# Kernel optimization log

Measured on AMD Instinct MI355X. Metric: run time of the kernel, lower is better.

Reference implementation:

```python
import jax, jax.numpy as jnp
import numpy as np

ALPHA = 0.1  # LeakyReLU slope

def _leaky(v):
    return jnp.where(v >= 0, v, ALPHA * v)

def setup_inputs() -> dict:
    key = jax.random.key(0)
    k1, k2, k3 = jax.random.split(key, 3)
    B, D_IN, D1, D2 = 262144, 200, 150, 100
    x = jax.random.normal(k1, (B, D_IN), dtype=jnp.float32)
    W1 = jax.random.normal(k2, (D_IN, D1), dtype=jnp.float32) * 0.05
    b1 = jnp.zeros((D1,), dtype=jnp.float32)
    W2 = jax.random.normal(k3, (D1, D2), dtype=jnp.float32) * 0.05
    b2 = jnp.zeros((D2,), dtype=jnp.float32)
    return {"x": x, "W1": W1, "b1": b1, "W2": W2, "b2": b2}

def reference(x, W1, b1, W2, b2):
    # Original loops per sample: dense(200->150)+LeakyReLU, mean -> out1;
    # dense(150->100)+LeakyReLU, mean -> out2. Batched here as single GEMMs.
    h1 = _leaky(x @ W1 + b1)           # [B, 150]
    out1 = jnp.mean(h1, axis=-1)       # [B]
    h2 = _leaky(h1 @ W2 + b2)          # [B, 100]
    out2 = jnp.mean(h2, axis=-1)       # [B]
    return (out1, out2)
```

## Files before the change

### kernel.cpp

```cpp
#include <hip/hip_runtime.h>

typedef unsigned short u16;
typedef unsigned int u32;
typedef __bf16 bf16x8 __attribute__((ext_vector_type(8)));
typedef float f32x4 __attribute__((ext_vector_type(4)));

#define W2F_OFF 71680
#define B1_OFF 107520
#define B2_OFF 108160
#define WS_BYTES 108608

__device__ __align__(256) unsigned char g_wbuf[WS_BYTES];

__device__ __forceinline__ u16 f2bf(float f) {
  __bf16 b = (__bf16)f;
  return __builtin_bit_cast(u16, b);
}
__device__ __forceinline__ u32 pk2bf(float a, float b) {
  return (u32)f2bf(a) | ((u32)f2bf(b) << 16);
}

__global__ void prep_kernel(const float* __restrict__ W1, const float* __restrict__ b1,
                            const float* __restrict__ W2, const float* __restrict__ b2)
{
  const int stride = gridDim.x * blockDim.x;
  const int tid0 = blockIdx.x * blockDim.x + threadIdx.x;
  u16* w1f = (u16*)g_wbuf;
  for (int e = tid0; e < 35840; e += stride) {
    int j = e & 7, l = (e >> 3) & 63, nt = (e >> 9) % 10, kt = e / 5120;
    int k = kt * 32 + ((l >> 4) << 3) + j;
    int n = nt * 16 + (l & 15);
    w1f[e] = (k < 200 && n < 150) ? f2bf(W1[k * 150 + n]) : (u16)0;
  }
  u16* w2f = (u16*)(g_wbuf + W2F_OFF);
  for (int e = tid0; e < 17920; e += stride) {
    int j = e & 7, l = (e >> 3) & 63, nt = (e >> 9) % 7, kt = e / 3584;
    int k = kt * 32 + ((l >> 4) << 3) + j;
    int n = nt * 16 + (l & 15);
    w2f[e] = (k < 150 && n < 100) ? f2bf(W2[k * 100 + n]) : (u16)0;
  }
  float* b1p = (float*)(g_wbuf + B1_OFF);
  for (int e = tid0; e < 160; e += stride) b1p[e] = (e < 150) ? b1[e] : 0.f;
  float* b2p = (float*)(g_wbuf + B2_OFF);
  for (int e = tid0; e < 112; e += stride) b2p[e] = (e < 100) ? b2[e] : 0.f;
}

__global__ __launch_bounds__(256, 5)
void fused_mlp(const float* __restrict__ x, float* __restrict__ out, int B)
{
  __shared__ __align__(16) u16 xs[12800];
  __shared__ float ps[2][2][64];

  const int tid = threadIdx.x;
  const int lane = tid & 63;
  const int wv = tid >> 6;
  const int h = wv & 1;
  const int pr = wv >> 1;
  const int cl = lane & 15, gr = lane >> 4;
  const long r0 = (long)blockIdx.x * 64;

  const u16* w1g = (const u16*)g_wbuf;
  const u16* w2g = (const u16*)(g_wbuf + W2F_OFF);

  const float* xg = x + r0 * 200;
  #pragma unroll
  for (int i = 0; i < 13; ++i) {
    int c = tid + i * 256;
    if (c < 3200) {
      int row = c / 50, kc = c % 50;
      float4 v = *reinterpret_cast<const float4*>(xg + row * 200 + kc * 4);
      int k0 = kc * 4;
      int mt = row >> 4;
      int idx;
      if (k0 < 192) {
        int F = mt * 6 + (k0 >> 5);
        int fl = (row & 15) | (((k0 & 31) >> 3) << 4);
        int slot = fl ^ (F & 7);
        idx = (F * 64 + slot) * 8 + (k0 & 7);
      } else {
        idx = 12288 + mt * 128 + (row & 15) * 8 + (k0 - 192);
      }
      uint2 p;
      p.x = pk2bf(v.x, v.y);
      p.y = pk2bf(v.z, v.w);
      *reinterpret_cast<uint2*>(&xs[idx]) = p;
    }
  }

  bf16x8 bfr[5];
  #pragma unroll
  for (int nt = 0; nt < 5; ++nt)
    bfr[nt] = *reinterpret_cast<const bf16x8*>(w1g + ((0 * 10 + 5 * h + nt) * 64 + lane) * 8);

  __syncthreads();

  const int mt0 = pr * 2, mt1 = pr * 2 + 1;
  const f32x4 zz = {0.f, 0.f, 0.f, 0.f};
  f32x4 acc1[2][5];
  #pragma unroll
  for (int i = 0; i < 2; ++i)
    #pragma unroll
    for (int nt = 0; nt < 5; ++nt) acc1[i][nt] = zz;

  #pragma unroll
  for (int kt = 0; kt < 7; ++kt) {
    bf16x8 a0, a1;
    if (kt < 6) {
      int F0 = mt0 * 6 + kt, F1 = mt1 * 6 + kt;
      a0 = *reinterpret_cast<const bf16x8*>(&xs[(F0 * 64 + (lane ^ (F0 & 7))) * 8]);
      a1 = *reinterpret_cast<const bf16x8*>(&xs[(F1 * 64 + (lane ^ (F1 & 7))) * 8]);
    } else {
      union { bf16x8 v; u32 w[4]; } A0, A1;
      A0.v = *reinterpret_cast<const bf16x8*>(&xs[12288 + mt0 * 128 + cl * 8]);
      A1.v = *reinterpret_cast<const bf16x8*>(&xs[12288 + mt1 * 128 + cl * 8]);
      if (gr != 0) {
        A0.w[0] = A0.w[1] = A0.w[2] = A0.w[3] = 0u;
        A1.w[0] = A1.w[1] = A1.w[2] = A1.w[3] = 0u;
      }
      a0 = A0.v; a1 = A1.v;
    }
    #pragma unroll
    for (int nt = 0; nt < 5; ++nt) {
      bf16x8 b = (kt == 0) ? bfr[nt]
        : *reinterpret_cast<const bf16x8*>(w1g + ((kt * 10 + 5 * h + nt) * 64 + lane) * 8);
      acc1[0][nt] = __builtin_amdgcn_mfma_f32_16x16x32_bf16(a0, b, acc1[0][nt], 0, 0, 0);
      acc1[1][nt] = __builtin_amdgcn_mfma_f32_16x16x32_bf16(a1, b, acc1[1][nt], 0, 0, 0);
    }
  }
  __syncthreads();

  const float* b1p = (const float*)(g_wbuf + B1_OFF);
  float b1v[5];
  #pragma unroll
  for (int nt = 0; nt < 5; ++nt) b1v[nt] = b1p[(5 * h + nt) * 16 + cl];

  float rs0[4] = {0, 0, 0, 0}, rs1[4] = {0, 0, 0, 0};
  #pragma unroll
  for (int nt = 0; nt < 5; ++nt) {
    int k2 = (5 * h + nt) * 16 + cl;
    int kt2 = k2 >> 5;
    int l2base = 16 * ((k2 & 31) >> 3);
    int e2 = k2 & 7;
    #pragma unroll
    for (int j = 0; j < 4; ++j) {
      int l2 = gr * 4 + j + l2base;
      float hv = acc1[0][nt][j] + b1v[nt];
      hv = (hv >= 0.f) ? hv : 0.1f * hv;
      rs0[j] += hv;
      xs[((mt0 * 5 + kt2) * 64 + l2) * 8 + e2] = f2bf(hv);
      float gv = acc1[1][nt][j] + b1v[nt];
      gv = (gv >= 0.f) ? gv : 0.1f * gv;
      rs1[j] += gv;
      xs[((mt1 * 5 + kt2) * 64 + l2) * 8 + e2] = f2bf(gv);
    }
  }
  #pragma unroll
  for (int j = 0; j < 4; ++j) {
    float s0 = rs0[j], s1 = rs1[j];
    #pragma unroll
    for (int mask = 1; mask < 16; mask <<= 1) {
      s0 += __shfl_xor(s0, mask, 64);
      s1 += __shfl_xor(s1, mask, 64);
    }
    if (cl == 0) {
      ps[0][h][mt0 * 16 + gr * 4 + j] = s0;
      ps[0][h][mt1 * 16 + gr * 4 + j] = s1;
    }
  }
  __syncthreads();

  if (wv == 0)
    out[r0 + lane] = (ps[0][0][lane] + ps[0][1][lane]) * (1.f / 150.f);

  f32x4 acc2[2][4];
  #pragma unroll
  for (int i = 0; i < 2; ++i)
    #pragma unroll
    for (int nt = 0; nt < 4; ++nt) acc2[i][nt] = zz;

  #pragma unroll
  for (int kt = 0; kt < 5; ++kt) {
    bf16x8 a0 = *reinterpret_cast<const bf16x8*>(&xs[((mt0 * 5 + kt) * 64 + lane) * 8]);
    bf16x8 a1 = *reinterpret_cast<const bf16x8*>(&xs[((mt1 * 5 + kt) * 64 + lane) * 8]);
    #pragma unroll
    for (int nt = 0; nt < 4; ++nt) {
      if (nt < 3 || h == 0) {
        bf16x8 b = *reinterpret_cast<const bf16x8*>(w2g + ((kt * 7 + 4 * h + nt) * 64 + lane) * 8);
        acc2[0][nt] = __builtin_amdgcn_mfma_f32_16x16x32_bf16(a0, b, acc2[0][nt], 0, 0, 0);
        acc2[1][nt] = __builtin_amdgcn_mfma_f32_16x16x32_bf16(a1, b, acc2[1][nt], 0, 0, 0);
      }
    }
  }

  const float* b2p = (const float*)(g_wbuf + B2_OFF);
  float b2v[4];
  #pragma unroll
  for (int nt = 0; nt < 4; ++nt)
    b2v[nt] = (nt < 3 || h == 0) ? b2p[(4 * h + nt) * 16 + cl] : 0.f;

  float t0[4] = {0, 0, 0, 0}, t1[4] = {0, 0, 0, 0};
  #pragma unroll
  for (int nt = 0; nt < 4; ++nt) {
    if (nt < 3 || h == 0) {
      #pragma unroll
      for (int j = 0; j < 4; ++j) {
        float hv = acc2[0][nt][j] + b2v[nt];
        hv = (hv >= 0.f) ? hv : 0.1f * hv;
        t0[j] += hv;
        float gv = acc2[1][nt][j] + b2v[nt];
        gv = (gv >= 0.f) ? gv : 0.1f * gv;
        t1[j] += gv;
      }
    }
  }
  #pragma unroll
  for (int j = 0; j < 4; ++j) {
    float s0 = t0[j], s1 = t1[j];
    #pragma unroll
    for (int mask = 1; mask < 16; mask <<= 1) {
      s0 += __shfl_xor(s0, mask, 64);
      s1 += __shfl_xor(s1, mask, 64);
    }
    if (cl == 0) {
      ps[1][h][mt0 * 16 + gr * 4 + j] = s0;
      ps[1][h][mt1 * 16 + gr * 4 + j] = s1;
    }
  }
  __syncthreads();

  if (wv == 0)
    out[B + r0 + lane] = (ps[1][0][lane] + ps[1][1][lane]) * (1.f / 100.f);
}

extern "C" void kernel_launch(void* const* d_in, const int* in_sizes, int n_in,
                              void* d_out, int out_size, void* d_ws, size_t ws_size,
                              hipStream_t stream)
{
  const float* x  = (const float*)d_in[0];
  const float* W1 = (const float*)d_in[1];
  const float* b1 = (const float*)d_in[2];
  const float* W2 = (const float*)d_in[3];
  const float* b2 = (const float*)d_in[4];
  float* out = (float*)d_out;
  const int B = in_sizes[0] / 200;

  prep_kernel<<<64, 256, 0, stream>>>(W1, b1, W2, b2);
  fused_mlp<<<B / 64, 256, 0, stream>>>(x, out, B);
}
```

Measured before the change: 80.41 us.

## Make fused MLP blocks loop over eight row tiles with LDS weights and prefetch

After: 88.87 us. 10.5% more time.

```diff
diff --git a/kernel.cpp b/kernel.cpp
--- a/kernel.cpp
+++ b/kernel.cpp
@@ -45,191 +45,196 @@
   for (int e = tid0; e < 112; e += stride) b2p[e] = (e < 100) ? b2[e] : 0.f;
 }
 
-__global__ __launch_bounds__(256, 5)
+__device__ __forceinline__ void stage_write(u16* __restrict__ xs, int c, float4 v) {
+  int row = c / 50, kc = c % 50;
+  int k0 = kc * 4, mt = row >> 4;
+  int idx;
+  if (k0 < 192) {
+    int F = mt * 6 + (k0 >> 5);
+    int fl = (row & 15) | (((k0 & 31) >> 3) << 4);
+    idx = (F * 64 + (fl ^ (F & 7))) * 8 + (k0 & 7);
+  } else {
+    idx = 12288 + mt * 128 + (row & 15) * 8 + (k0 - 192);
+  }
+  uint2 p;
+  p.x = pk2bf(v.x, v.y);
+  p.y = pk2bf(v.z, v.w);
+  *reinterpret_cast<uint2*>(&xs[idx]) = p;
+}
+
+#define NT 8
+#define SMEM_BYTES 159744
+
+__global__ __launch_bounds__(512, 2)
 void fused_mlp(const float* __restrict__ x, float* __restrict__ out, int B)
 {
-  __shared__ __align__(16) u16 xs[12800];
-  __shared__ float ps[2][2][64];
+  extern __shared__ __align__(16) u16 smem[];
+  u16* wlds = smem;
+  float* ps = (float*)(smem + 79360);
 
   const int tid = threadIdx.x;
   const int lane = tid & 63;
   const int wv = tid >> 6;
   const int h = wv & 1;
-  const int pr = wv >> 1;
+  const int mt = wv >> 1;
   const int cl = lane & 15, gr = lane >> 4;
-  const long r0 = (long)blockIdx.x * 64;
-
-  const u16* w1g = (const u16*)g_wbuf;
-  const u16* w2g = (const u16*)(g_wbuf + W2F_OFF);
-
-  const float* xg = x + r0 * 200;
-  #pragma unroll
-  for (int i = 0; i < 13; ++i) {
-    int c = tid + i * 256;
-    if (c < 3200) {
-      int row = c / 50, kc = c % 50;
-      float4 v = *reinterpret_cast<const float4*>(xg + row * 200 + kc * 4);
-      int k0 = kc * 4;
-      int mt = row >> 4;
-      int idx;
-      if (k0 < 192) {
-        int F = mt * 6 + (k0 >> 5);
-        int fl = (row & 15) | (((k0 & 31) >> 3) << 4);
-        int slot = fl ^ (F & 7);
-        idx = (F * 64 + slot) * 8 + (k0 & 7);
-      } else {
-        idx = 12288 + mt * 128 + (row & 15) * 8 + (k0 - 192);
-      }
-      uint2 p;
-      p.x = pk2bf(v.x, v.y);
-      p.y = pk2bf(v.z, v.w);
-      *reinterpret_cast<uint2*>(&xs[idx]) = p;
-    }
-  }
-
-  bf16x8 bfr[5];
-  #pragma unroll
-  for (int nt = 0; nt < 5; ++nt)
-    bfr[nt] = *reinterpret_cast<const bf16x8*>(w1g + ((0 * 10 + 5 * h + nt) * 64 + lane) * 8);
-
-  __syncthreads();
-
-  const int mt0 = pr * 2, mt1 = pr * 2 + 1;
-  const f32x4 zz = {0.f, 0.f, 0.f, 0.f};
-  f32x4 acc1[2][5];
-  #pragma unroll
-  for (int i = 0; i < 2; ++i)
-    #pragma unroll
-    for (int nt = 0; nt < 5; ++nt) acc1[i][nt] = zz;
-
-  #pragma unroll
-  for (int kt = 0; kt < 7; ++kt) {
-    bf16x8 a0, a1;
-    if (kt < 6) {
-      int F0 = mt0 * 6 + kt, F1 = mt1 * 6 + kt;
-      a0 = *reinterpret_cast<const bf16x8*>(&xs[(F0 * 64 + (lane ^ (F0 & 7))) * 8]);
-      a1 = *reinterpret_cast<const bf16x8*>(&xs[(F1 * 64 + (lane ^ (F1 & 7))) * 8]);
-    } else {
-      union { bf16x8 v; u32 w[4]; } A0, A1;
-      A0.v = *reinterpret_cast<const bf16x8*>(&xs[12288 + mt0 * 128 + cl * 8]);
-      A1.v = *reinterpret_cast<const bf16x8*>(&xs[12288 + mt1 * 128 + cl * 8]);
-      if (gr != 0) {
-        A0.w[0] = A0.w[1] = A0.w[2] = A0.w[3] = 0u;
-        A1.w[0] = A1.w[1] = A1.w[2] = A1.w[3] = 0u;
-      }
-      a0 = A0.v; a1 = A1.v;
-    }
-    #pragma unroll
-    for (int nt = 0; nt < 5; ++nt) {
-      bf16x8 b = (kt == 0) ? bfr[nt]
-        : *reinterpret_cast<const bf16x8*>(w1g + ((kt * 10 + 5 * h + nt) * 64 + lane) * 8);
-      acc1[0][nt] = __builtin_amdgcn_mfma_f32_16x16x32_bf16(a0, b, acc1[0][nt], 0, 0, 0);
-      acc1[1][nt] = __builtin_amdgcn_mfma_f32_16x16x32_bf16(a1, b, acc1[1][nt], 0, 0, 0);
-    }
-  }
-  __syncthreads();
+
+  {
+    const uint4* src = (const uint4*)g_wbuf;
+    uint4* dst = (uint4*)wlds;
+    #pragma unroll
+    for (int i = 0; i < 14; ++i) {
+      int c = tid + i * 512;
+      if (c < 6720) dst[c] = src[c];
+    }
+  }
 
   const float* b1p = (const float*)(g_wbuf + B1_OFF);
+  const float* b2p = (const float*)(g_wbuf + B2_OFF);
   float b1v[5];
   #pragma unroll
   for (int nt = 0; nt < 5; ++nt) b1v[nt] = b1p[(5 * h + nt) * 16 + cl];
-
-  float rs0[4] = {0, 0, 0, 0}, rs1[4] = {0, 0, 0, 0};
-  #pragma unroll
-  for (int nt = 0; nt < 5; ++nt) {
-    int k2 = (5 * h + nt) * 16 + cl;
-    int kt2 = k2 >> 5;
-    int l2base = 16 * ((k2 & 31) >> 3);
-    int e2 = k2 & 7;
-    #pragma unroll
-    for (int j = 0; j < 4; ++j) {
-      int l2 = gr * 4 + j + l2base;
-      float hv = acc1[0][nt][j] + b1v[nt];
-      hv = (hv >= 0.f) ? hv : 0.1f * hv;
-      rs0[j] += hv;
-      xs[((mt0 * 5 + kt2) * 64 + l2) * 8 + e2] = f2bf(hv);
-      float gv = acc1[1][nt][j] + b1v[nt];
-      gv = (gv >= 0.f) ? gv : 0.1f * gv;
-      rs1[j] += gv;
-      xs[((mt1 * 5 + kt2) * 64 + l2) * 8 + e2] = f2bf(gv);
-    }
-  }
-  #pragma unroll
-  for (int j = 0; j < 4; ++j) {
-    float s0 = rs0[j], s1 = rs1[j];
-    #pragma unroll
-    for (int mask = 1; mask < 16; mask <<= 1) {
-      s0 += __shfl_xor(s0, mask, 64);
-      s1 += __shfl_xor(s1, mask, 64);
-    }
-    if (cl == 0) {
-      ps[0][h][mt0 * 16 + gr * 4 + j] = s0;
-      ps[0][h][mt1 * 16 + gr * 4 + j] = s1;
-    }
-  }
-  __syncthreads();
-
-  if (wv == 0)
-    out[r0 + lane] = (ps[0][0][lane] + ps[0][1][lane]) * (1.f / 150.f);
-
-  f32x4 acc2[2][4];
-  #pragma unroll
-  for (int i = 0; i < 2; ++i)
-    #pragma unroll
-    for (int nt = 0; nt < 4; ++nt) acc2[i][nt] = zz;
-
-  #pragma unroll
-  for (int kt = 0; kt < 5; ++kt) {
-    bf16x8 a0 = *reinterpret_cast<const bf16x8*>(&xs[((mt0 * 5 + kt) * 64 + lane) * 8]);
-    bf16x8 a1 = *reinterpret_cast<const bf16x8*>(&xs[((mt1 * 5 + kt) * 64 + lane) * 8]);
-    #pragma unroll
-    for (int nt = 0; nt < 4; ++nt) {
-      if (nt < 3 || h == 0) {
-        bf16x8 b = *reinterpret_cast<const bf16x8*>(w2g + ((kt * 7 + 4 * h + nt) * 64 + lane) * 8);
-        acc2[0][nt] = __builtin_amdgcn_mfma_f32_16x16x32_bf16(a0, b, acc2[0][nt], 0, 0, 0);
-        acc2[1][nt] = __builtin_amdgcn_mfma_f32_16x16x32_bf16(a1, b, acc2[1][nt], 0, 0, 0);
-      }
-    }
-  }
-
-  const float* b2p = (const float*)(g_wbuf + B2_OFF);
   float b2v[4];
   #pragma unroll
   for (int nt = 0; nt < 4; ++nt)
     b2v[nt] = (nt < 3 || h == 0) ? b2p[(4 * h + nt) * 16 + cl] : 0.f;
 
-  float t0[4] = {0, 0, 0, 0}, t1[4] = {0, 0, 0, 0};
-  #pragma unroll
-  for (int nt = 0; nt < 4; ++nt) {
-    if (nt < 3 || h == 0) {
+  const long rowBase = (long)blockIdx.x * (NT * 64);
+  const f32x4 zz = {0.f, 0.f, 0.f, 0.f};
+
+  float4 rv[7];
+  {
+    const float* xg = x + rowBase * 200;
+    #pragma unroll
+    for (int i = 0; i < 7; ++i) {
+      int c = tid + i * 512;
+      rv[i] = (c < 3200) ? *reinterpret_cast<const float4*>(xg + (c / 50) * 200 + (c % 50) * 4)
+                         : make_float4(0.f, 0.f, 0.f, 0.f);
+    }
+    u16* x0 = smem + 53760;
+    #pragma unroll
+    for (int i = 0; i < 7; ++i) {
+      int c = tid + i * 512;
+      if (c < 3200) stage_write(x0, c, rv[i]);
+    }
+  }
+  __syncthreads();
+
+  for (int t = 0; t < NT; ++t) {
+    u16* xcur = smem + 53760 + (t & 1) * 12800;
+    u16* xnxt = smem + 53760 + ((t + 1) & 1) * 12800;
+    const long r0t = rowBase + (long)t * 64;
+
+    if (t + 1 < NT) {
+      const float* xg = x + (r0t + 64) * 200;
+      #pragma unroll
+      for (int i = 0; i < 7; ++i) {
+        int c = tid + i * 512;
+        rv[i] = (c < 3200) ? *reinterpret_cast<const float4*>(xg + (c / 50) * 200 + (c % 50) * 4)
+                           : make_float4(0.f, 0.f, 0.f, 0.f);
+      }
+    }
+
+    f32x4 acc1[5];
+    #pragma unroll
+    for (int nt = 0; nt < 5; ++nt) acc1[nt] = zz;
+
+    #pragma unroll
+    for (int kt = 0; kt < 7; ++kt) {
+      bf16x8 a;
+      if (kt < 6) {
+        int F = mt * 6 + kt;
+        a = *reinterpret_cast<const bf16x8*>(&xcur[(F * 64 + (lane ^ (F & 7))) * 8]);
+      } else {
+        union { bf16x8 v; u32 w[4]; } A;
+        A.v = *reinterpret_cast<const bf16x8*>(&xcur[12288 + mt * 128 + cl * 8]);
+        if (gr != 0) { A.w[0] = A.w[1] = A.w[2] = A.w[3] = 0u; }
+        a = A.v;
+      }
+      #pragma unroll
+      for (int nt = 0; nt < 5; ++nt) {
+        bf16x8 b = *reinterpret_cast<const bf16x8*>(&wlds[((kt * 10 + 5 * h + nt) * 64 + lane) * 8]);
+        acc1[nt] = __builtin_amdgcn_mfma_f32_16x16x32_bf16(a, b, acc1[nt], 0, 0, 0);
+      }
+    }
+    __syncthreads();
+
+    float rs[4] = {0, 0, 0, 0};
+    #pragma unroll
+    for (int nt = 0; nt < 5; ++nt) {
+      int k2 = (5 * h + nt) * 16 + cl;
+      int kt2 = k2 >> 5;
+      int l2base = 16 * ((k2 & 31) >> 3);
+      int e2 = k2 & 7;
       #pragma unroll
       for (int j = 0; j < 4; ++j) {
-        float hv = acc2[0][nt][j] + b2v[nt];
+        int l2 = gr * 4 + j + l2base;
+        float hv = acc1[nt][j] + b1v[nt];
         hv = (hv >= 0.f) ? hv : 0.1f * hv;
-        t0[j] += hv;
-        float gv = acc2[1][nt][j] + b2v[nt];
-        gv = (gv >= 0.f) ? gv : 0.1f * gv;
-        t1[j] += gv;
-      }
-    }
-  }
-  #pragma unroll
-  for (int j = 0; j < 4; ++j) {
-    float s0 = t0[j], s1 = t1[j];
-    #pragma unroll
-    for (int mask = 1; mask < 16; mask <<= 1) {
-      s0 += __shfl_xor(s0, mask, 64);
-      s1 += __shfl_xor(s1, mask, 64);
-    }
-    if (cl == 0) {
-      ps[1][h][mt0 * 16 + gr * 4 + j] = s0;
-      ps[1][h][mt1 * 16 + gr * 4 + j] = s1;
-    }
-  }
-  __syncthreads();
-
-  if (wv == 0)
-    out[B + r0 + lane] = (ps[1][0][lane] + ps[1][1][lane]) * (1.f / 100.f);
+        rs[j] += hv;
+        xcur[((mt * 5 + kt2) * 64 + l2) * 8 + e2] = f2bf(hv);
+      }
+    }
+    #pragma unroll
+    for (int j = 0; j < 4; ++j) {
+      float s = rs[j];
+      #pragma unroll
+      for (int mask = 1; mask < 16; mask <<= 1) s += __shfl_xor(s, mask, 64);
+      if (cl == 0) ps[h * 64 + mt * 16 + gr * 4 + j] = s;
+    }
+    __syncthreads();
+
+    if (tid < 64)
+      out[r0t + tid] = (ps[tid] + ps[64 + tid]) * (1.f / 150.f);
+
+    f32x4 acc2[4];
+    #pragma unroll
+    for (int nt = 0; nt < 4; ++nt) acc2[nt] = zz;
+
+    #pragma unroll
+    for (int kt = 0; kt < 5; ++kt) {
+      bf16x8 a = *reinterpret_cast<const bf16x8*>(&xcur[((mt * 5 + kt) * 64 + lane) * 8]);
+      #pragma unroll
+      for (int nt = 0; nt < 4; ++nt) {
+        if (nt < 3 || h == 0) {
+          bf16x8 b = *reinterpret_cast<const bf16x8*>(&wlds[35840 + ((kt * 7 + 4 * h + nt) * 64 + lane) * 8]);
+          acc2[nt] = __builtin_amdgcn_mfma_f32_16x16x32_bf16(a, b, acc2[nt], 0, 0, 0);
+        }
+      }
+    }
+
+    float ts[4] = {0, 0, 0, 0};
+    #pragma unroll
+    for (int nt = 0; nt < 4; ++nt) {
+      if (nt < 3 || h == 0) {
+        #pragma unroll
+        for (int j = 0; j < 4; ++j) {
+          float hv = acc2[nt][j] + b2v[nt];
+          hv = (hv >= 0.f) ? hv : 0.1f * hv;
+          ts[j] += hv;
+        }
+      }
+    }
+    #pragma unroll
+    for (int j = 0; j < 4; ++j) {
+      float s = ts[j];
+      #pragma unroll
+      for (int mask = 1; mask < 16; mask <<= 1) s += __shfl_xor(s, mask, 64);
+      if (cl == 0) ps[128 + h * 64 + mt * 16 + gr * 4 + j] = s;
+    }
+
+    if (t + 1 < NT) {
+      #pragma unroll
+      for (int i = 0; i < 7; ++i) {
+        int c = tid + i * 512;
+        if (c < 3200) stage_write(xnxt, c, rv[i]);
+      }
+    }
+    __syncthreads();
+
+    if (tid < 64)
+      out[B + r0t + tid] = (ps[128 + tid] + ps[192 + tid]) * (1.f / 100.f);
+  }
 }
 
 extern "C" void kernel_launch(void* const* d_in, const int* in_sizes, int n_in,
@@ -244,6 +249,9 @@
   float* out = (float*)d_out;
   const int B = in_sizes[0] / 200;
 
+  hipFuncSetAttribute(reinterpret_cast<const void*>(fused_mlp),
+                      hipFuncAttributeMaxDynamicSharedMemorySize, SMEM_BYTES);
+
   prep_kernel<<<64, 256, 0, stream>>>(W1, b1, W2, b2);
-  fused_mlp<<<B / 64, 256, 0, stream>>>(x, out, B);
-}
+  fused_mlp<<<B / (NT * 64), 512, SMEM_BYTES, stream>>>(x, out, B);
+}
```

## Stage weight tiles into LDS via double-buffered global_load_lds

Applied to the files above, without the earlier changes.

Result: slower. 91.27 us (+13.5%).

```diff
diff --git a/kernel.cpp b/kernel.cpp
--- a/kernel.cpp
+++ b/kernel.cpp
@@ -18,6 +18,12 @@
 }
 __device__ __forceinline__ u32 pk2bf(float a, float b) {
   return (u32)f2bf(a) | ((u32)f2bf(b) << 16);
+}
+
+typedef __attribute__((address_space(1))) const u32 gas_u32;
+typedef __attribute__((address_space(3))) u32 las_u32;
+__device__ __forceinline__ void gl16(const void* g, void* l) {
+  __builtin_amdgcn_global_load_lds((gas_u32*)g, (las_u32*)l, 16, 0, 0);
 }
 
 __global__ void prep_kernel(const float* __restrict__ W1, const float* __restrict__ b1,
@@ -45,10 +51,11 @@
   for (int e = tid0; e < 112; e += stride) b2p[e] = (e < 100) ? b2[e] : 0.f;
 }
 
-__global__ __launch_bounds__(256, 5)
+__global__ __launch_bounds__(256, 3)
 void fused_mlp(const float* __restrict__ x, float* __restrict__ out, int B)
 {
   __shared__ __align__(16) u16 xs[12800];
+  __shared__ __align__(16) u16 wbuf[2][5120];
   __shared__ float ps[2][2][64];
 
   const int tid = threadIdx.x;
@@ -59,8 +66,11 @@
   const int cl = lane & 15, gr = lane >> 4;
   const long r0 = (long)blockIdx.x * 64;
 
-  const u16* w1g = (const u16*)g_wbuf;
-  const u16* w2g = (const u16*)(g_wbuf + W2F_OFF);
+  const char* w1g = (const char*)g_wbuf;
+  const char* w2g = (const char*)g_wbuf + W2F_OFF;
+
+  for (int f = wv; f < 10; f += 4)
+    gl16(w1g + f * 1024 + lane * 16, (char*)&wbuf[0][0] + f * 1024);
 
   const float* xg = x + r0 * 200;
   #pragma unroll
@@ -75,8 +85,7 @@
       if (k0 < 192) {
         int F = mt * 6 + (k0 >> 5);
         int fl = (row & 15) | (((k0 & 31) >> 3) << 4);
-        int slot = fl ^ (F & 7);
-        idx = (F * 64 + slot) * 8 + (k0 & 7);
+        idx = (F * 64 + (fl ^ (F & 7))) * 8 + (k0 & 7);
       } else {
         idx = 12288 + mt * 128 + (row & 15) * 8 + (k0 - 192);
       }
@@ -86,12 +95,6 @@
       *reinterpret_cast<uint2*>(&xs[idx]) = p;
     }
   }
-
-  bf16x8 bfr[5];
-  #pragma unroll
-  for (int nt = 0; nt < 5; ++nt)
-    bfr[nt] = *reinterpret_cast<const bf16x8*>(w1g + ((0 * 10 + 5 * h + nt) * 64 + lane) * 8);
-
   __syncthreads();
 
   const int mt0 = pr * 2, mt1 = pr * 2 + 1;
@@ -104,6 +107,13 @@
 
   #pragma unroll
   for (int kt = 0; kt < 7; ++kt) {
+    {
+      const char* src = (kt < 6) ? (w1g + (kt + 1) * 10240) : w2g;
+      const int nf = (kt < 6) ? 10 : 7;
+      char* dst = (char*)&wbuf[(kt + 1) & 1][0];
+      for (int f = wv; f < nf; f += 4)
+        gl16(src + f * 1024 + lane * 16, dst + f * 1024);
+    }
     bf16x8 a0, a1;
     if (kt < 6) {
       int F0 = mt0 * 6 + kt, F1 = mt1 * 6 + kt;
@@ -119,15 +129,15 @@
       }
       a0 = A0.v; a1 = A1.v;
     }
+    const u16* wb = &wbuf[kt & 1][0];
     #pragma unroll
     for (int nt = 0; nt < 5; ++nt) {
-      bf16x8 b = (kt == 0) ? bfr[nt]
-        : *reinterpret_cast<const bf16x8*>(w1g + ((kt * 10 + 5 * h + nt) * 64 + lane) * 8);
+      bf16x8 b = *reinterpret_cast<const bf16x8*>(&wb[(5 * h + nt) * 512 + lane * 8]);
       acc1[0][nt] = __builtin_amdgcn_mfma_f32_16x16x32_bf16(a0, b, acc1[0][nt], 0, 0, 0);
       acc1[1][nt] = __builtin_amdgcn_mfma_f32_16x16x32_bf16(a1, b, acc1[1][nt], 0, 0, 0);
     }
-  }
-  __syncthreads();
+    __syncthreads();
+  }
 
   const float* b1p = (const float*)(g_wbuf + B1_OFF);
   float b1v[5];
@@ -169,8 +179,8 @@
   }
   __syncthreads();
 
-  if (wv == 0)
-    out[r0 + lane] = (ps[0][0][lane] + ps[0][1][lane]) * (1.f / 150.f);
+  if (tid < 64)
+    out[r0 + tid] = (ps[0][0][tid] + ps[0][1][tid]) * (1.f / 150.f);
 
   f32x4 acc2[2][4];
   #pragma unroll
@@ -180,16 +190,24 @@
 
   #pragma unroll
   for (int kt = 0; kt < 5; ++kt) {
+    if (kt < 4) {
+      const char* src = w2g + (kt + 1) * 7168;
+      char* dst = (char*)&wbuf[kt & 1][0];
+      for (int f = wv; f < 7; f += 4)
+        gl16(src + f * 1024 + lane * 16, dst + f * 1024);
+    }
     bf16x8 a0 = *reinterpret_cast<const bf16x8*>(&xs[((mt0 * 5 + kt) * 64 + lane) * 8]);
     bf16x8 a1 = *reinterpret_cast<const bf16x8*>(&xs[((mt1 * 5 + kt) * 64 + lane) * 8]);
+    const u16* wb = &wbuf[(kt + 1) & 1][0];
     #pragma unroll
     for (int nt = 0; nt < 4; ++nt) {
       if (nt < 3 || h == 0) {
-        bf16x8 b = *reinterpret_cast<const bf16x8*>(w2g + ((kt * 7 + 4 * h + nt) * 64 + lane) * 8);
+        bf16x8 b = *reinterpret_cast<const bf16x8*>(&wb[(4 * h + nt) * 512 + lane * 8]);
         acc2[0][nt] = __builtin_amdgcn_mfma_f32_16x16x32_bf16(a0, b, acc2[0][nt], 0, 0, 0);
         acc2[1][nt] = __builtin_amdgcn_mfma_f32_16x16x32_bf16(a1, b, acc2[1][nt], 0, 0, 0);
       }
     }
+    if (kt < 4) __syncthreads();
   }
 
   const float* b2p = (const float*)(g_wbuf + B2_OFF);
@@ -228,8 +246,8 @@
   }
   __syncthreads();
 
-  if (wv == 0)
-    out[B + r0 + lane] = (ps[1][0][lane] + ps[1][1][lane]) * (1.f / 100.f);
+  if (tid < 64)
+    out[B + r0 + tid] = (ps[1][0][tid] + ps[1][1][tid]) * (1.f / 100.f);
 }
 
 extern "C" void kernel_launch(void* const* d_in, const int* in_sizes, int n_in,
```
